# Kernel tuning notes

Hardware: AMD Instinct MI355X
Metric: run time of the kernel (lower is better)

The kernel has to match this reference:

```python
import jax, jax.numpy as jnp
import numpy as np

B, N, DEG = 64, 512, 16        # graphs, nodes per graph, avg degree
C, HID = 10, 128               # input feat dim (== num_classes quirk), hidden
E = B * N * DEG                # total edges (fixed; pooling masks edges)


def _gcn(x, W, b, src, dst, emask, n):
    # PyG GCNConv: add self-loops, symmetric norm D^-1/2 (A+I) D^-1/2 (XW) + b
    h = x @ W
    deg = jax.ops.segment_sum(emask, dst, num_segments=n) + 1.0  # +1 self-loop
    dinv = jax.lax.rsqrt(deg)
    norm = dinv[src] * dinv[dst] * emask
    agg = jax.ops.segment_sum(h[src] * norm[:, None], dst, num_segments=n)
    return agg + h * (dinv * dinv)[:, None] + b  # self-loop term + bias


def _sag_pool(x, src, dst, emask, Wp, bp, n_per):
    # SAGPooling: score = tanh(GCN(x)); per-graph top-k (ratio=0.5); x' = x[perm]*score
    n = x.shape[0]
    score = jnp.tanh(_gcn(x, Wp, bp, src, dst, emask, n)[:, 0])
    k = n_per // 2
    vals, idx = jax.lax.top_k(score.reshape(B, n_per), k)  # [B,k]
    perm = (idx + (jnp.arange(B) * n_per)[:, None]).reshape(-1)
    xk = x[perm] * vals.reshape(-1)[:, None]
    # relabel edges; drop edges touching removed nodes via mask (fixed E)
    mapping = jnp.full((n,), -1, jnp.int32).at[perm].set(
        jnp.arange(B * k, dtype=jnp.int32))
    ns, nd = mapping[src], mapping[dst]
    nmask = emask * ((ns >= 0) & (nd >= 0)).astype(emask.dtype)
    return xk, jnp.maximum(ns, 0), jnp.maximum(nd, 0), nmask, k


def _readout(x, k):
    # global max pool || global mean pool (all kept nodes are real, no padding)
    xg = x.reshape(B, k, -1)
    return jnp.concatenate([xg.max(axis=1), xg.mean(axis=1)], axis=1)


def setup_inputs() -> dict:
    key = jax.random.key(0)
    ks = jax.random.split(key, 16)
    x = jax.random.normal(ks[0], (B * N, C), jnp.float32)
    off = jnp.repeat(jnp.arange(B, dtype=jnp.int32) * N, N * DEG)
    src = jax.random.randint(ks[1], (E,), 0, N, jnp.int32) + off
    dst = jax.random.randint(ks[2], (E,), 0, N, jnp.int32) + off
    p = lambda k, s: jax.random.normal(k, s, jnp.float32) * 0.05
    return {
        "x": x, "src": src, "dst": dst,
        "W1": p(ks[3], (C, HID)), "b1": jnp.zeros((HID,), jnp.float32),
        "W2": p(ks[4], (HID, HID)), "b2": jnp.zeros((HID,), jnp.float32),
        "W3": p(ks[5], (HID, HID)), "b3": jnp.zeros((HID,), jnp.float32),
        "Wp": p(ks[6], (HID, 1)), "bp": jnp.zeros((1,), jnp.float32),
        "L1W": p(ks[7], (2 * HID, HID)), "L1b": jnp.zeros((HID,), jnp.float32),
        "L2W": p(ks[8], (HID, HID // 2)), "L2b": jnp.zeros((HID // 2,), jnp.float32),
    }


def reference(x, src, dst, W1, b1, W2, b2, W3, b3, Wp, bp, L1W, L1b, L2W, L2b):
    emask = jnp.ones((E,), jnp.float32)
    h = jax.nn.relu(_gcn(x, W1, b1, src, dst, emask, B * N))
    h, src, dst, emask, k = _sag_pool(h, src, dst, emask, Wp, bp, N)
    x1 = _readout(h, k)
    h = jax.nn.relu(_gcn(h, W2, b2, src, dst, emask, B * k))
    h, src, dst, emask, k = _sag_pool(h, src, dst, emask, Wp, bp, k)
    x2 = _readout(h, k)
    h = jax.nn.relu(_gcn(h, W3, b3, src, dst, emask, B * k))
    h, src, dst, emask, k = _sag_pool(h, src, dst, emask, Wp, bp, k)
    x3 = _readout(h, k)
    z = x1 + x2 + x3
    z = jax.nn.relu(z @ L1W + L1b)
    # dropout inactive in eval mode
    z = jax.nn.relu(z @ L2W + L2b)
    return jax.nn.log_softmax(z, axis=1)
```

## Files before the change

kernel.cpp:

```cpp
#include <hip/hip_runtime.h>
#include <math.h>

#define BGR 64
#define N0 512
#define E_TOT (BGR*N0*16)
#define EPG 8192
#define EIT 16
#define HID 128


__global__ __launch_bounds__(512) void k_topo0(
    const int* __restrict__ s0, const int* __restrict__ d0,
    int2* __restrict__ edges, int* __restrict__ cnt, int* __restrict__ rowptr,
    float* __restrict__ dinv, int2* __restrict__ csr){
  __shared__ int   deg[512];
  __shared__ int   sb[512];
  __shared__ int   cur[512];
  __shared__ float dl[512];
  int g = (blockIdx.x & 7)*8 + (blockIdx.x >> 3);
  int t = threadIdx.x;
  int gbase = g*N0, ebase = g*EPG;
  deg[t] = 0;
  __syncthreads();
  int2 ebuf[EIT];
  #pragma unroll
  for (int it = 0; it < EIT; it++){
    int i = ebase + it*512 + t;
    int2 e = make_int2(s0[i], d0[i]);
    ebuf[it] = e;
    edges[i] = e;
    atomicAdd(&deg[e.y - gbase], 1);
  }
  __syncthreads();
  int vdeg = deg[t];
  sb[t] = vdeg; __syncthreads();
  for (int off = 1; off < 512; off <<= 1){
    int add = (t >= off) ? sb[t-off] : 0;
    __syncthreads(); sb[t] += add; __syncthreads();
  }
  int excl = sb[t] - vdeg;
  rowptr[gbase + t] = ebase + excl;
  cnt[gbase + t] = vdeg;
  cur[t] = excl;
  float dv = rsqrtf((float)vdeg + 1.f);
  dl[t] = dv;
  dinv[gbase + t] = dv;
  __syncthreads();
  #pragma unroll
  for (int it = 0; it < EIT; it++){
    int2 e = ebuf[it];
    int sl = e.x - gbase, dc = e.y - gbase;
    int pos = atomicAdd(&cur[dc], 1);
    csr[ebase + pos] = make_int2(e.x, __float_as_int(dl[sl]*dl[dc]));
  }
}

__global__ __launch_bounds__(512) void k_l1_fused(
    const float* __restrict__ x, const float* __restrict__ W1,
    const int2* __restrict__ csr, const int* __restrict__ rowptr,
    const int* __restrict__ cnt, const float* __restrict__ dinv,
    const float* __restrict__ b1, const float* __restrict__ Wp,
    float4* __restrict__ gout4, float* __restrict__ hp_part){
  extern __shared__ float hl[];
  int b = blockIdx.x;
  int xcd = b & 7, idx = b >> 3;
  int graph = xcd*8 + (idx >> 3);
  int sub = idx & 7;
  int qf = sub >> 1, half = sub & 1;
  int t = threadIdx.x;
  int gbase = graph*N0;
  int fp = t & 31;
  int f = qf*32 + fp;
  float wcol[10];
  #pragma unroll
  for (int k = 0; k < 10; k++) wcol[k] = W1[k*HID + f];
  for (int n = t >> 5; n < N0; n += 16){
    const float* xr = x + (gbase + n)*10;
    float acc = 0.f;
    #pragma unroll
    for (int k = 0; k < 10; k++) acc += xr[k]*wcol[k];
    hl[n*32 + fp] = acc;
  }
  __syncthreads();
  const float4* hl4 = (const float4*)hl;
  int l = t & 7, grp = t >> 3;
  float4 bb = ((const float4*)b1)[qf*8 + l];
  float4 wp = ((const float4*)Wp)[qf*8 + l];
  int n0 = half*256;
  for (int nl = n0 + grp; nl < n0 + 256; nl += 64){
    int node = gbase + nl;
    int start = rowptr[node], c = cnt[node];
    float4 acc = make_float4(0.f,0.f,0.f,0.f);
    int j = 0;
    for (; j + 4 <= c; j += 4){
      int2 e0 = csr[start+j],   e1 = csr[start+j+1];
      int2 e2 = csr[start+j+2], e3 = csr[start+j+3];
      float4 h0 = hl4[(e0.x - gbase)*8 + l];
      float4 h1 = hl4[(e1.x - gbase)*8 + l];
      float4 h2 = hl4[(e2.x - gbase)*8 + l];
      float4 h3 = hl4[(e3.x - gbase)*8 + l];
      float w0 = __int_as_float(e0.y), w1 = __int_as_float(e1.y);
      float w2 = __int_as_float(e2.y), w3 = __int_as_float(e3.y);
      acc.x += w0*h0.x + w1*h1.x + w2*h2.x + w3*h3.x;
      acc.y += w0*h0.y + w1*h1.y + w2*h2.y + w3*h3.y;
      acc.z += w0*h0.z + w1*h1.z + w2*h2.z + w3*h3.z;
      acc.w += w0*h0.w + w1*h1.w + w2*h2.w + w3*h3.w;
    }
    for (; j < c; j++){
      int2 e = csr[start + j];
      float wgt = __int_as_float(e.y);
      float4 hv = hl4[(e.x - gbase)*8 + l];
      acc.x += wgt*hv.x; acc.y += wgt*hv.y; acc.z += wgt*hv.z; acc.w += wgt*hv.w;
    }
    float di = dinv[node], dd = di*di;
    float4 hs = hl4[nl*8 + l];
    float4 v;
    v.x = fmaxf(acc.x + hs.x*dd + bb.x, 0.f);
    v.y = fmaxf(acc.y + hs.y*dd + bb.y, 0.f);
    v.z = fmaxf(acc.z + hs.z*dd + bb.z, 0.f);
    v.w = fmaxf(acc.w + hs.w*dd + bb.w, 0.f);
    gout4[node*32 + qf*8 + l] = v;
    float contrib = v.x*wp.x + v.y*wp.y + v.z*wp.z + v.w*wp.w;
    #pragma unroll
    for (int off = 4; off; off >>= 1) contrib += __shfl_down(contrib, off, 8);
    if (l == 0) hp_part[qf*32768 + node] = contrib;
  }
}

__global__ void k_gemm16(const float* __restrict__ x, const float* __restrict__ W,
                         float* __restrict__ out, int nper){
  __shared__ float xr[16][HID];
  int b = blockIdx.x;
  int xcd = b & 7, idx = b >> 3, bpg = nper >> 4;
  int graph = xcd*8 + idx / bpg;
  int base = graph*nper + (idx % bpg)*16;
  int f = threadIdx.x;
  #pragma unroll
  for (int nd = 0; nd < 16; nd++) xr[nd][f] = x[(base+nd)*HID + f];
  __syncthreads();
  float acc[16];
  #pragma unroll
  for (int nd = 0; nd < 16; nd++) acc[nd] = 0.f;
  for (int i = 0; i < HID; i++){
    float wv = W[i*HID + f];
    #pragma unroll
    for (int nd = 0; nd < 16; nd++) acc[nd] += xr[nd][i]*wv;
  }
  #pragma unroll
  for (int nd = 0; nd < 16; nd++) out[(base+nd)*HID + f] = acc[nd];
}

__global__ __launch_bounds__(256) void k_gcn_gather(
    const float4* __restrict__ h4, const int2* __restrict__ csr,
    const int* __restrict__ rowptr, const int* __restrict__ cnt,
    const float* __restrict__ dinv, const float4* __restrict__ bias4,
    const float4* __restrict__ Wp4, float4* __restrict__ out4,
    float* __restrict__ hp, int nper){
  int b = blockIdx.x;
  int xcd = b & 7, idx = b >> 3, bpg = nper >> 3;
  int graph = xcd*8 + idx / bpg;
  int node = graph*nper + (idx % bpg)*8 + (threadIdx.x >> 5);
  int l = threadIdx.x & 31;
  int start = rowptr[node], c = cnt[node];
  float4 acc = make_float4(0.f, 0.f, 0.f, 0.f);
  int j = 0;
  for (; j + 4 <= c; j += 4){
    int2 e0 = csr[start+j],   e1 = csr[start+j+1];
    int2 e2 = csr[start+j+2], e3 = csr[start+j+3];
    float4 h0 = h4[e0.x*32 + l];
    float4 h1 = h4[e1.x*32 + l];
    float4 h2 = h4[e2.x*32 + l];
    float4 h3 = h4[e3.x*32 + l];
    float w0 = __int_as_float(e0.y), w1 = __int_as_float(e1.y);
    float w2 = __int_as_float(e2.y), w3 = __int_as_float(e3.y);
    acc.x += w0*h0.x + w1*h1.x + w2*h2.x + w3*h3.x;
    acc.y += w0*h0.y + w1*h1.y + w2*h2.y + w3*h3.y;
    acc.z += w0*h0.z + w1*h1.z + w2*h2.z + w3*h3.z;
    acc.w += w0*h0.w + w1*h1.w + w2*h2.w + w3*h3.w;
  }
  for (; j < c; j++){
    int2 e = csr[start + j];
    float wgt = __int_as_float(e.y);
    float4 hv = h4[e.x*32 + l];
    acc.x += wgt*hv.x; acc.y += wgt*hv.y; acc.z += wgt*hv.z; acc.w += wgt*hv.w;
  }
  float di = dinv[node], dd = di*di;
  float4 hs = h4[node*32 + l];
  float4 bb = bias4[l];
  float4 v;
  v.x = fmaxf(acc.x + hs.x*dd + bb.x, 0.f);
  v.y = fmaxf(acc.y + hs.y*dd + bb.y, 0.f);
  v.z = fmaxf(acc.z + hs.z*dd + bb.z, 0.f);
  v.w = fmaxf(acc.w + hs.w*dd + bb.w, 0.f);
  out4[node*32 + l] = v;
  float4 wp = Wp4[l];
  float contrib = v.x*wp.x + v.y*wp.y + v.z*wp.z + v.w*wp.w;
  #pragma unroll
  for (int off = 16; off; off >>= 1) contrib += __shfl_down(contrib, off, 32);
  if (l == 0) hp[node] = contrib;
}

__global__ __launch_bounds__(512) void k_mega(
    const float4* __restrict__ gout4, const float* __restrict__ hp_part,
    int l1flag, const float* __restrict__ hp,
    int2* __restrict__ csr, int* __restrict__ rowptr, int* __restrict__ cnt,
    float* __restrict__ dinv, const float* __restrict__ bp,
    int2* __restrict__ edges, float4* __restrict__ xpool4,
    float* __restrict__ z, int nper, int lastlev,
    const float* __restrict__ L1W, const float* __restrict__ L1b,
    const float* __restrict__ L2W, const float* __restrict__ L2b,
    float* __restrict__ out){
  __shared__ float sv[512];
  __shared__ int   si[512];
  __shared__ float hpl[512];
  __shared__ int   map[512];
  __shared__ int   sb[512];
  __shared__ int   cur[256];
  __shared__ float dl[256];
  __shared__ float4 pmx[16][32];
  __shared__ float4 psm[16][32];
  __shared__ float zr[256];
  __shared__ float h1[128];
  __shared__ float h2[64];
  __shared__ float red[2];
  int g = (blockIdx.x & 7)*8 + (blockIdx.x >> 3);
  int t = threadIdx.x;
  int k = nper >> 1;
  int gbase = g*nper, ebase = g*EPG, gb2 = g*k;
  bool act = t < nper;
  if (act){
    int node = gbase + t;
    hpl[t] = l1flag ? (hp_part[node] + hp_part[32768 + node] +
                       hp_part[65536 + node] + hp_part[98304 + node])
                    : hp[node];
  }
  __syncthreads();
  float v = 0.f; int idx = t;
  if (act){
    int start = rowptr[gbase + t], c = cnt[gbase + t];
    float a = 0.f;
    int j = 0;
    for (; j + 4 <= c; j += 4){
      int2 e0 = csr[start+j],   e1 = csr[start+j+1];
      int2 e2 = csr[start+j+2], e3 = csr[start+j+3];
      a += __int_as_float(e0.y)*hpl[e0.x - gbase]
         + __int_as_float(e1.y)*hpl[e1.x - gbase]
         + __int_as_float(e2.y)*hpl[e2.x - gbase]
         + __int_as_float(e3.y)*hpl[e3.x - gbase];
    }
    for (; j < c; j++){
      int2 e = csr[start + j];
      a += __int_as_float(e.y)*hpl[e.x - gbase];
    }
    float di = dinv[gbase + t];
    v = tanhf(a + hpl[t]*di*di + bp[0]);
  }
  for (int kk = 2; kk <= nper; kk <<= 1){
    for (int jj = kk >> 1; jj > 0; jj >>= 1){
      if (jj >= 64){
        if (act){ sv[t] = v; si[t] = idx; }
        __syncthreads();
        if (act){
          int p = t ^ jj;
          float pv = sv[p]; int pi = si[p];
          bool amLower = (t & jj) == 0;
          bool dirDesc = (t & kk) == 0;
          bool betterMine = (v > pv) || (v == pv && idx < pi);
          if ((amLower == dirDesc) != betterMine){ v = pv; idx = pi; }
        }
        __syncthreads();
      } else if (act){
        float pv = __shfl_xor(v, jj);
        int   pi = __shfl_xor(idx, jj);
        bool amLower = (t & jj) == 0;
        bool dirDesc = (t & kk) == 0;
        bool betterMine = (v > pv) || (v == pv && idx < pi);
        if ((amLower == dirDesc) != betterMine){ v = pv; idx = pi; }
      }
    }
  }
  if (act){ sv[t] = v; si[t] = idx; }
  __syncthreads();
  int l = t & 31, j0 = t >> 5;
  float4 mx = make_float4(-INFINITY,-INFINITY,-INFINITY,-INFINITY);
  float4 sm = make_float4(0.f,0.f,0.f,0.f);
  for (int j = j0; j < k; j += 16){
    float val = sv[j]; int row = si[j];
    float4 hv = gout4[(gbase + row)*32 + l];
    float4 o = make_float4(hv.x*val, hv.y*val, hv.z*val, hv.w*val);
    if (!lastlev) xpool4[(gb2 + j)*32 + l] = o;
    mx.x = fmaxf(mx.x, o.x); mx.y = fmaxf(mx.y, o.y);
    mx.z = fmaxf(mx.z, o.z); mx.w = fmaxf(mx.w, o.w);
    sm.x += o.x; sm.y += o.y; sm.z += o.z; sm.w += o.w;
  }
  pmx[j0][l] = mx; psm[j0][l] = sm;
  __syncthreads();
  if (t < 32){
    float4 M = pmx[0][t], S = psm[0][t];
    #pragma unroll
    for (int q = 1; q < 16; q++){
      float4 m2 = pmx[q][t], s2 = psm[q][t];
      M.x = fmaxf(M.x, m2.x); M.y = fmaxf(M.y, m2.y);
      M.z = fmaxf(M.z, m2.z); M.w = fmaxf(M.w, m2.w);
      S.x += s2.x; S.y += s2.y; S.z += s2.z; S.w += s2.w;
    }
    float ki = 1.f/(float)k;
    float* zp = z + g*256;
    if (l1flag){
      zp[t*4+0] = M.x; zp[t*4+1] = M.y; zp[t*4+2] = M.z; zp[t*4+3] = M.w;
      zp[128+t*4+0] = S.x*ki; zp[128+t*4+1] = S.y*ki;
      zp[128+t*4+2] = S.z*ki; zp[128+t*4+3] = S.w*ki;
    } else if (!lastlev){
      zp[t*4+0] += M.x; zp[t*4+1] += M.y; zp[t*4+2] += M.z; zp[t*4+3] += M.w;
      zp[128+t*4+0] += S.x*ki; zp[128+t*4+1] += S.y*ki;
      zp[128+t*4+2] += S.z*ki; zp[128+t*4+3] += S.w*ki;
    } else {
      zr[t*4+0] = zp[t*4+0] + M.x; zr[t*4+1] = zp[t*4+1] + M.y;
      zr[t*4+2] = zp[t*4+2] + M.z; zr[t*4+3] = zp[t*4+3] + M.w;
      zr[128+t*4+0] = zp[128+t*4+0] + S.x*ki;
      zr[128+t*4+1] = zp[128+t*4+1] + S.y*ki;
      zr[128+t*4+2] = zp[128+t*4+2] + S.z*ki;
      zr[128+t*4+3] = zp[128+t*4+3] + S.w*ki;
    }
  }
  if (lastlev){
    __syncthreads();
    if (t < 128){
      float a = L1b[t];
      for (int i = 0; i < 256; i++) a += zr[i]*L1W[i*128 + t];
      h1[t] = fmaxf(a, 0.f);
    }
    __syncthreads();
    if (t < 64){
      float a = L2b[t];
      for (int i = 0; i < 128; i++) a += h1[i]*L2W[i*64 + t];
      h2[t] = fmaxf(a, 0.f);
    }
    __syncthreads();
    if (t == 0){
      float mxv = -INFINITY;
      for (int i = 0; i < 64; i++) mxv = fmaxf(mxv, h2[i]);
      float s = 0.f;
      for (int i = 0; i < 64; i++) s += expf(h2[i] - mxv);
      red[0] = mxv; red[1] = logf(s);
    }
    __syncthreads();
    if (t < 64) out[g*64 + t] = h2[t] - red[0] - red[1];
    return;
  }
  if (act) map[t] = -1;
  if (t < k) sb[t] = 0;
  __syncthreads();
  if (t < k) map[si[t]] = t;
  __syncthreads();
  int2 ebuf[EIT];
  #pragma unroll
  for (int it = 0; it < EIT; it++){
    int i = ebase + it*512 + t;
    int2 e = edges[i];
    int2 ne = make_int2(-1, 0);
    if (e.x >= 0){
      int ns = map[e.x - gbase], nd = map[e.y - gbase];
      if (ns >= 0 && nd >= 0){
        ne = make_int2(gb2 + ns, gb2 + nd);
        atomicAdd(&sb[nd], 1);
      }
    }
    ebuf[it] = ne;
    edges[i] = ne;
  }
  __syncthreads();
  int vdeg = (t < k) ? sb[t] : 0;
  for (int off = 1; off < k; off <<= 1){
    int add = (t >= off && t < k) ? sb[t-off] : 0;
    __syncthreads();
    if (t < k) sb[t] += add;
    __syncthreads();
  }
  if (t < k){
    int excl = sb[t] - vdeg;
    rowptr[gb2 + t] = ebase + excl;
    cnt[gb2 + t] = vdeg;
    cur[t] = excl;
    float dv = rsqrtf((float)vdeg + 1.f);
    dl[t] = dv;
    dinv[gb2 + t] = dv;
  }
  __syncthreads();
  #pragma unroll
  for (int it = 0; it < EIT; it++){
    int2 e = ebuf[it];
    if (e.x >= 0){
      int sl = e.x - gb2, dc = e.y - gb2;
      int pos = atomicAdd(&cur[dc], 1);
      csr[ebase + pos] = make_int2(e.x, __float_as_int(dl[sl]*dl[dc]));
    }
  }
}

extern "C" void kernel_launch(void* const* d_in, const int* in_sizes, int n_in,
                              void* d_out, int out_size, void* d_ws, size_t ws_size,
                              hipStream_t stream){
  (void)in_sizes; (void)n_in; (void)out_size; (void)ws_size;
  const float* x0  = (const float*)d_in[0];
  const int*   s0  = (const int*)  d_in[1];
  const int*   d0  = (const int*)  d_in[2];
  const float* W1  = (const float*)d_in[3];  const float* b1 = (const float*)d_in[4];
  const float* W2  = (const float*)d_in[5];  const float* b2 = (const float*)d_in[6];
  const float* W3  = (const float*)d_in[7];  const float* b3 = (const float*)d_in[8];
  const float* Wp  = (const float*)d_in[9];  const float* bp = (const float*)d_in[10];
  const float* L1W = (const float*)d_in[11]; const float* L1b = (const float*)d_in[12];
  const float* L2W = (const float*)d_in[13]; const float* L2b = (const float*)d_in[14];
  float* out = (float*)d_out;

  float* w = (float*)d_ws;
  float* h     = w; w += 32768*HID;
  float* gout  = w; w += 32768*HID;
  float* xpA   = h    + 16384*HID;
  float* xpB   = gout + 16384*HID;
  float* xpC   = xpA;
  float* dinvv = w; w += 32768;
  float* hp    = w; w += 32768;
  float* hppt  = w; w += 4*32768;
  float* z     = w; w += BGR*256;
  int* cnt     = (int*)w; w += 32768;
  int* rowptr  = (int*)w; w += 32768;
  int2* edges  = (int2*)w; w += 2*E_TOT;
  int2* csr    = (int2*)w; w += 2*E_TOT;

  k_topo0<<<BGR, 512, 0, stream>>>(s0, d0, edges, cnt, rowptr, dinvv, csr);

  k_l1_fused<<<512, 512, 65536, stream>>>(x0, W1, csr, rowptr, cnt, dinvv,
                                          b1, Wp, (float4*)gout, hppt);
  k_mega<<<BGR, 512, 0, stream>>>((const float4*)gout, hppt, 1, hp, csr, rowptr,
                                  cnt, dinvv, bp, edges, (float4*)xpA, z, 512, 0,
                                  L1W, L1b, L2W, L2b, out);
  k_gemm16<<<16384/16, HID, 0, stream>>>(xpA, W2, h, 256);
  k_gcn_gather<<<16384/8, 256, 0, stream>>>((const float4*)h, csr, rowptr, cnt,
                                            dinvv, (const float4*)b2,
                                            (const float4*)Wp, (float4*)gout,
                                            hp, 256);
  k_mega<<<BGR, 512, 0, stream>>>((const float4*)gout, hppt, 0, hp, csr, rowptr,
                                  cnt, dinvv, bp, edges, (float4*)xpB, z, 256, 0,
                                  L1W, L1b, L2W, L2b, out);
  k_gemm16<<<8192/16, HID, 0, stream>>>(xpB, W3, h, 128);
  k_gcn_gather<<<8192/8, 256, 0, stream>>>((const float4*)h, csr, rowptr, cnt,
                                           dinvv, (const float4*)b3,
                                           (const float4*)Wp, (float4*)gout,
                                           hp, 128);
  k_mega<<<BGR, 512, 0, stream>>>((const float4*)gout, hppt, 0, hp, csr, rowptr,
                                  cnt, dinvv, bp, edges, (float4*)xpC, z, 128, 1,
                                  L1W, L1b, L2W, L2b, out);
}
```

Baseline: 246.0 us.

## Fuse pooling levels 2-3, GEMMs and readout into one per-graph tail kernel

Replaces the seven launches after layer 1 (three pooling kernels, two GEMMs, two gathers) with one kernel that runs one 512-thread block per graph. Each block keeps pooled features in 128 KB of LDS and does the GEMM, GCN aggregation, scoring, sort, relabel and readout in place, using coherent atomic loads for CSR data it rewrote itself. This removes launch overhead and global round-trips of intermediate features. In exchange only 64 blocks run, so most of the GPU sits idle during the dense GEMM and gather stages, and the large LDS footprint limits occupancy.

Result: slower. 268.0 us (+9.0%).

```diff
diff --git a/kernel.cpp b/kernel.cpp
--- a/kernel.cpp
+++ b/kernel.cpp
@@ -8,6 +8,186 @@
 #define EIT 16
 #define HID 128
 
+
+__device__ __forceinline__ int2 ldcoh(const int2* p){
+  unsigned long long v = __hip_atomic_load(
+      (const unsigned long long*)p, __ATOMIC_RELAXED, __HIP_MEMORY_SCOPE_AGENT);
+  int2 r; r.x = (int)(unsigned int)v; r.y = (int)(unsigned int)(v >> 32);
+  return r;
+}
+
+template<bool COH>
+__device__ __forceinline__ int2 lde(const int2* p){
+  if (COH) return ldcoh(p);
+  return *p;
+}
+
+template<bool COH>
+__device__ __forceinline__ float score_edges(const int2* __restrict__ csr,
+    int start, int c, const float* hloc, int gbase){
+  float a = 0.f; int j = 0;
+  for (; j + 4 <= c; j += 4){
+    int2 e0 = lde<COH>(csr+start+j),   e1 = lde<COH>(csr+start+j+1);
+    int2 e2 = lde<COH>(csr+start+j+2), e3 = lde<COH>(csr+start+j+3);
+    a += __int_as_float(e0.y)*hloc[e0.x - gbase]
+       + __int_as_float(e1.y)*hloc[e1.x - gbase]
+       + __int_as_float(e2.y)*hloc[e2.x - gbase]
+       + __int_as_float(e3.y)*hloc[e3.x - gbase];
+  }
+  for (; j < c; j++){
+    int2 e = lde<COH>(csr+start+j);
+    a += __int_as_float(e.y)*hloc[e.x - gbase];
+  }
+  return a;
+}
+
+__device__ __forceinline__ float4 row_edges_coh(const int2* __restrict__ csr,
+    int start, int c, const float4* h4, int gbase, int l){
+  float4 acc = make_float4(0.f,0.f,0.f,0.f);
+  int j = 0;
+  for (; j + 4 <= c; j += 4){
+    int2 e0 = ldcoh(csr+start+j),   e1 = ldcoh(csr+start+j+1);
+    int2 e2 = ldcoh(csr+start+j+2), e3 = ldcoh(csr+start+j+3);
+    float4 h0 = h4[(e0.x - gbase)*32 + l];
+    float4 h1 = h4[(e1.x - gbase)*32 + l];
+    float4 h2 = h4[(e2.x - gbase)*32 + l];
+    float4 h3 = h4[(e3.x - gbase)*32 + l];
+    float w0 = __int_as_float(e0.y), w1 = __int_as_float(e1.y);
+    float w2 = __int_as_float(e2.y), w3 = __int_as_float(e3.y);
+    acc.x += w0*h0.x + w1*h1.x + w2*h2.x + w3*h3.x;
+    acc.y += w0*h0.y + w1*h1.y + w2*h2.y + w3*h3.y;
+    acc.z += w0*h0.z + w1*h1.z + w2*h2.z + w3*h3.z;
+    acc.w += w0*h0.w + w1*h1.w + w2*h2.w + w3*h3.w;
+  }
+  for (; j < c; j++){
+    int2 e = ldcoh(csr+start+j);
+    float wgt = __int_as_float(e.y);
+    float4 hv = h4[(e.x - gbase)*32 + l];
+    acc.x += wgt*hv.x; acc.y += wgt*hv.y; acc.z += wgt*hv.z; acc.w += wgt*hv.w;
+  }
+  return acc;
+}
+
+__device__ __forceinline__ void bitonic_sort(float* sv, int* si, float v, int idx,
+                                             int t, int nper, bool act){
+  for (int kk = 2; kk <= nper; kk <<= 1){
+    for (int jj = kk >> 1; jj > 0; jj >>= 1){
+      if (jj >= 64){
+        if (act){ sv[t] = v; si[t] = idx; }
+        __syncthreads();
+        if (act){
+          int p = t ^ jj;
+          float pv = sv[p]; int pi = si[p];
+          bool amLower = (t & jj) == 0;
+          bool dirDesc = (t & kk) == 0;
+          bool betterMine = (v > pv) || (v == pv && idx < pi);
+          if ((amLower == dirDesc) != betterMine){ v = pv; idx = pi; }
+        }
+        __syncthreads();
+      } else if (act){
+        float pv = __shfl_xor(v, jj);
+        int   pi = __shfl_xor(idx, jj);
+        bool amLower = (t & jj) == 0;
+        bool dirDesc = (t & kk) == 0;
+        bool betterMine = (v > pv) || (v == pv && idx < pi);
+        if ((amLower == dirDesc) != betterMine){ v = pv; idx = pi; }
+      }
+    }
+  }
+  if (act){ sv[t] = v; si[t] = idx; }
+  __syncthreads();
+}
+
+template<bool COH>
+__device__ __forceinline__ void relabel(int2* __restrict__ edges,
+    int2* __restrict__ csr, const int* si, int* map, int* sb, int* cur,
+    float* dl, int* rpl, int* cntl, int t, int nper, int k,
+    int gbase, int ebase){
+  if (t < nper) map[t] = -1;
+  if (t < k) sb[t] = 0;
+  __syncthreads();
+  if (t < k) map[si[t]] = t;
+  __syncthreads();
+  int2 ebuf[EIT];
+  #pragma unroll
+  for (int it = 0; it < EIT; it++){
+    int i = ebase + it*512 + t;
+    int2 e = lde<COH>(edges + i);
+    int2 ne = make_int2(-1, 0);
+    if (e.x >= 0){
+      int ns = map[e.x - gbase], nd = map[e.y - gbase];
+      if (ns >= 0 && nd >= 0){
+        ne = make_int2(gbase + ns, gbase + nd);
+        atomicAdd(&sb[nd], 1);
+      }
+    }
+    ebuf[it] = ne;
+    edges[i] = ne;
+  }
+  __syncthreads();
+  int vdeg = (t < k) ? sb[t] : 0;
+  for (int off = 1; off < k; off <<= 1){
+    int add = (t >= off && t < k) ? sb[t-off] : 0;
+    __syncthreads();
+    if (t < k) sb[t] += add;
+    __syncthreads();
+  }
+  if (t < k){
+    int excl = sb[t] - vdeg;
+    rpl[t] = ebase + excl;
+    cntl[t] = vdeg;
+    cur[t] = excl;
+    float dv = rsqrtf((float)vdeg + 1.f);
+    dl[t] = dv;
+  }
+  __syncthreads();
+  #pragma unroll
+  for (int it = 0; it < EIT; it++){
+    int2 e = ebuf[it];
+    if (e.x >= 0){
+      int sl = e.x - gbase, dc = e.y - gbase;
+      int pos = atomicAdd(&cur[dc], 1);
+      csr[ebase + pos] = make_int2(e.x, __float_as_int(dl[sl]*dl[dc]));
+    }
+  }
+  __syncthreads();
+}
+
+__device__ __forceinline__ void gemm_inplace(float* xl, const float* __restrict__ W,
+                                             int nn, int t){
+  float4* xl4 = (float4*)xl;
+  int fq = t & 31;
+  int ng = t >> 5;
+  for (int tb = 0; tb < nn; tb += 64){
+    int n0 = tb + ng*4;
+    float4 acc[4];
+    #pragma unroll
+    for (int c = 0; c < 4; c++) acc[c] = make_float4(0.f,0.f,0.f,0.f);
+    for (int i = 0; i < HID; i += 4){
+      float4 w0 = *(const float4*)(W + (i+0)*HID + fq*4);
+      float4 w1 = *(const float4*)(W + (i+1)*HID + fq*4);
+      float4 w2 = *(const float4*)(W + (i+2)*HID + fq*4);
+      float4 w3 = *(const float4*)(W + (i+3)*HID + fq*4);
+      #pragma unroll
+      for (int c = 0; c < 4; c++){
+        float4 xv = *(const float4*)(xl + (n0+c)*HID + i);
+        acc[c].x += xv.x*w0.x; acc[c].x += xv.y*w1.x;
+        acc[c].x += xv.z*w2.x; acc[c].x += xv.w*w3.x;
+        acc[c].y += xv.x*w0.y; acc[c].y += xv.y*w1.y;
+        acc[c].y += xv.z*w2.y; acc[c].y += xv.w*w3.y;
+        acc[c].z += xv.x*w0.z; acc[c].z += xv.y*w1.z;
+        acc[c].z += xv.z*w2.z; acc[c].z += xv.w*w3.z;
+        acc[c].w += xv.x*w0.w; acc[c].w += xv.y*w1.w;
+        acc[c].w += xv.z*w2.w; acc[c].w += xv.w*w3.w;
+      }
+    }
+    __syncthreads();
+    #pragma unroll
+    for (int c = 0; c < 4; c++)
+      xl4[(n0+c)*32 + fq] = acc[c];
+  }
+  __syncthreads();
+}
 
 __global__ __launch_bounds__(512) void k_topo0(
     const int* __restrict__ s0, const int* __restrict__ d0,
@@ -127,275 +307,252 @@
   }
 }
 
-__global__ void k_gemm16(const float* __restrict__ x, const float* __restrict__ W,
-                         float* __restrict__ out, int nper){
-  __shared__ float xr[16][HID];
-  int b = blockIdx.x;
-  int xcd = b & 7, idx = b >> 3, bpg = nper >> 4;
-  int graph = xcd*8 + idx / bpg;
-  int base = graph*nper + (idx % bpg)*16;
-  int f = threadIdx.x;
-  #pragma unroll
-  for (int nd = 0; nd < 16; nd++) xr[nd][f] = x[(base+nd)*HID + f];
-  __syncthreads();
-  float acc[16];
-  #pragma unroll
-  for (int nd = 0; nd < 16; nd++) acc[nd] = 0.f;
-  for (int i = 0; i < HID; i++){
-    float wv = W[i*HID + f];
-    #pragma unroll
-    for (int nd = 0; nd < 16; nd++) acc[nd] += xr[nd][i]*wv;
-  }
-  #pragma unroll
-  for (int nd = 0; nd < 16; nd++) out[(base+nd)*HID + f] = acc[nd];
-}
-
-__global__ __launch_bounds__(256) void k_gcn_gather(
-    const float4* __restrict__ h4, const int2* __restrict__ csr,
-    const int* __restrict__ rowptr, const int* __restrict__ cnt,
-    const float* __restrict__ dinv, const float4* __restrict__ bias4,
-    const float4* __restrict__ Wp4, float4* __restrict__ out4,
-    float* __restrict__ hp, int nper){
-  int b = blockIdx.x;
-  int xcd = b & 7, idx = b >> 3, bpg = nper >> 3;
-  int graph = xcd*8 + idx / bpg;
-  int node = graph*nper + (idx % bpg)*8 + (threadIdx.x >> 5);
-  int l = threadIdx.x & 31;
-  int start = rowptr[node], c = cnt[node];
-  float4 acc = make_float4(0.f, 0.f, 0.f, 0.f);
-  int j = 0;
-  for (; j + 4 <= c; j += 4){
-    int2 e0 = csr[start+j],   e1 = csr[start+j+1];
-    int2 e2 = csr[start+j+2], e3 = csr[start+j+3];
-    float4 h0 = h4[e0.x*32 + l];
-    float4 h1 = h4[e1.x*32 + l];
-    float4 h2 = h4[e2.x*32 + l];
-    float4 h3 = h4[e3.x*32 + l];
-    float w0 = __int_as_float(e0.y), w1 = __int_as_float(e1.y);
-    float w2 = __int_as_float(e2.y), w3 = __int_as_float(e3.y);
-    acc.x += w0*h0.x + w1*h1.x + w2*h2.x + w3*h3.x;
-    acc.y += w0*h0.y + w1*h1.y + w2*h2.y + w3*h3.y;
-    acc.z += w0*h0.z + w1*h1.z + w2*h2.z + w3*h3.z;
-    acc.w += w0*h0.w + w1*h1.w + w2*h2.w + w3*h3.w;
-  }
-  for (; j < c; j++){
-    int2 e = csr[start + j];
-    float wgt = __int_as_float(e.y);
-    float4 hv = h4[e.x*32 + l];
-    acc.x += wgt*hv.x; acc.y += wgt*hv.y; acc.z += wgt*hv.z; acc.w += wgt*hv.w;
-  }
-  float di = dinv[node], dd = di*di;
-  float4 hs = h4[node*32 + l];
-  float4 bb = bias4[l];
-  float4 v;
-  v.x = fmaxf(acc.x + hs.x*dd + bb.x, 0.f);
-  v.y = fmaxf(acc.y + hs.y*dd + bb.y, 0.f);
-  v.z = fmaxf(acc.z + hs.z*dd + bb.z, 0.f);
-  v.w = fmaxf(acc.w + hs.w*dd + bb.w, 0.f);
-  out4[node*32 + l] = v;
-  float4 wp = Wp4[l];
-  float contrib = v.x*wp.x + v.y*wp.y + v.z*wp.z + v.w*wp.w;
-  #pragma unroll
-  for (int off = 16; off; off >>= 1) contrib += __shfl_down(contrib, off, 32);
-  if (l == 0) hp[node] = contrib;
-}
-
-__global__ __launch_bounds__(512) void k_mega(
+__global__ __launch_bounds__(512) void k_tail(
     const float4* __restrict__ gout4, const float* __restrict__ hp_part,
-    int l1flag, const float* __restrict__ hp,
-    int2* __restrict__ csr, int* __restrict__ rowptr, int* __restrict__ cnt,
-    float* __restrict__ dinv, const float* __restrict__ bp,
-    int2* __restrict__ edges, float4* __restrict__ xpool4,
-    float* __restrict__ z, int nper, int lastlev,
+    int2* __restrict__ csr, int2* __restrict__ edges,
+    const int* __restrict__ rowptr1, const int* __restrict__ cnt1,
+    const float* __restrict__ dinv1, const float* __restrict__ bp,
+    const float* __restrict__ W2, const float* __restrict__ b2,
+    const float* __restrict__ W3, const float* __restrict__ b3,
+    const float* __restrict__ Wp,
     const float* __restrict__ L1W, const float* __restrict__ L1b,
     const float* __restrict__ L2W, const float* __restrict__ L2b,
     float* __restrict__ out){
+  __shared__ float xl[256*HID];
   __shared__ float sv[512];
   __shared__ int   si[512];
   __shared__ float hpl[512];
-  __shared__ int   map[512];
-  __shared__ int   sb[512];
-  __shared__ int   cur[256];
+  __shared__ union UU {
+    struct { int map[512]; int sb[512]; int cur[256]; } r;
+    float4 pr[2][16][32];
+  } u;
   __shared__ float dl[256];
-  __shared__ float4 pmx[16][32];
-  __shared__ float4 psm[16][32];
-  __shared__ float zr[256];
-  __shared__ float h1[128];
-  __shared__ float h2[64];
+  __shared__ int   rpl[256];
+  __shared__ int   cntl[256];
+  __shared__ float zacc[256];
   __shared__ float red[2];
+
   int g = (blockIdx.x & 7)*8 + (blockIdx.x >> 3);
   int t = threadIdx.x;
-  int k = nper >> 1;
-  int gbase = g*nper, ebase = g*EPG, gb2 = g*k;
-  bool act = t < nper;
-  if (act){
+  int gbase = g*N0, ebase = g*EPG;
+  int l = t & 31, j0 = t >> 5;
+  float4* xl4 = (float4*)xl;
+  float bp0 = bp[0];
+
+  {
     int node = gbase + t;
-    hpl[t] = l1flag ? (hp_part[node] + hp_part[32768 + node] +
-                       hp_part[65536 + node] + hp_part[98304 + node])
-                    : hp[node];
-  }
-  __syncthreads();
-  float v = 0.f; int idx = t;
-  if (act){
-    int start = rowptr[gbase + t], c = cnt[gbase + t];
-    float a = 0.f;
-    int j = 0;
-    for (; j + 4 <= c; j += 4){
-      int2 e0 = csr[start+j],   e1 = csr[start+j+1];
-      int2 e2 = csr[start+j+2], e3 = csr[start+j+3];
-      a += __int_as_float(e0.y)*hpl[e0.x - gbase]
-         + __int_as_float(e1.y)*hpl[e1.x - gbase]
-         + __int_as_float(e2.y)*hpl[e2.x - gbase]
-         + __int_as_float(e3.y)*hpl[e3.x - gbase];
-    }
-    for (; j < c; j++){
-      int2 e = csr[start + j];
-      a += __int_as_float(e.y)*hpl[e.x - gbase];
-    }
-    float di = dinv[gbase + t];
-    v = tanhf(a + hpl[t]*di*di + bp[0]);
-  }
-  for (int kk = 2; kk <= nper; kk <<= 1){
-    for (int jj = kk >> 1; jj > 0; jj >>= 1){
-      if (jj >= 64){
-        if (act){ sv[t] = v; si[t] = idx; }
-        __syncthreads();
-        if (act){
-          int p = t ^ jj;
-          float pv = sv[p]; int pi = si[p];
-          bool amLower = (t & jj) == 0;
-          bool dirDesc = (t & kk) == 0;
-          bool betterMine = (v > pv) || (v == pv && idx < pi);
-          if ((amLower == dirDesc) != betterMine){ v = pv; idx = pi; }
-        }
-        __syncthreads();
-      } else if (act){
-        float pv = __shfl_xor(v, jj);
-        int   pi = __shfl_xor(idx, jj);
-        bool amLower = (t & jj) == 0;
-        bool dirDesc = (t & kk) == 0;
-        bool betterMine = (v > pv) || (v == pv && idx < pi);
-        if ((amLower == dirDesc) != betterMine){ v = pv; idx = pi; }
+    hpl[t] = hp_part[node] + hp_part[32768 + node]
+           + hp_part[65536 + node] + hp_part[98304 + node];
+  }
+  __syncthreads();
+  {
+    int start = rowptr1[gbase + t], c = cnt1[gbase + t];
+    float a = score_edges<false>(csr, start, c, hpl, gbase);
+    float di = dinv1[gbase + t];
+    float v = tanhf(a + hpl[t]*di*di + bp0);
+    bitonic_sort(sv, si, v, t, t, 512, true);
+  }
+  {
+    float4 mx = make_float4(-INFINITY,-INFINITY,-INFINITY,-INFINITY);
+    float4 sm = make_float4(0.f,0.f,0.f,0.f);
+    for (int j = j0; j < 256; j += 16){
+      float val = sv[j]; int row = si[j];
+      float4 hv = gout4[(gbase + row)*32 + l];
+      float4 o = make_float4(hv.x*val, hv.y*val, hv.z*val, hv.w*val);
+      xl4[j*32 + l] = o;
+      mx.x = fmaxf(mx.x, o.x); mx.y = fmaxf(mx.y, o.y);
+      mx.z = fmaxf(mx.z, o.z); mx.w = fmaxf(mx.w, o.w);
+      sm.x += o.x; sm.y += o.y; sm.z += o.z; sm.w += o.w;
+    }
+    u.pr[0][j0][l] = mx; u.pr[1][j0][l] = sm;
+    __syncthreads();
+    if (t < 32){
+      float4 M = u.pr[0][0][t], S = u.pr[1][0][t];
+      #pragma unroll
+      for (int q = 1; q < 16; q++){
+        float4 m2 = u.pr[0][q][t], s2 = u.pr[1][q][t];
+        M.x = fmaxf(M.x, m2.x); M.y = fmaxf(M.y, m2.y);
+        M.z = fmaxf(M.z, m2.z); M.w = fmaxf(M.w, m2.w);
+        S.x += s2.x; S.y += s2.y; S.z += s2.z; S.w += s2.w;
       }
-    }
-  }
-  if (act){ sv[t] = v; si[t] = idx; }
-  __syncthreads();
-  int l = t & 31, j0 = t >> 5;
-  float4 mx = make_float4(-INFINITY,-INFINITY,-INFINITY,-INFINITY);
-  float4 sm = make_float4(0.f,0.f,0.f,0.f);
-  for (int j = j0; j < k; j += 16){
-    float val = sv[j]; int row = si[j];
-    float4 hv = gout4[(gbase + row)*32 + l];
-    float4 o = make_float4(hv.x*val, hv.y*val, hv.z*val, hv.w*val);
-    if (!lastlev) xpool4[(gb2 + j)*32 + l] = o;
-    mx.x = fmaxf(mx.x, o.x); mx.y = fmaxf(mx.y, o.y);
-    mx.z = fmaxf(mx.z, o.z); mx.w = fmaxf(mx.w, o.w);
-    sm.x += o.x; sm.y += o.y; sm.z += o.z; sm.w += o.w;
-  }
-  pmx[j0][l] = mx; psm[j0][l] = sm;
-  __syncthreads();
-  if (t < 32){
-    float4 M = pmx[0][t], S = psm[0][t];
-    #pragma unroll
-    for (int q = 1; q < 16; q++){
-      float4 m2 = pmx[q][t], s2 = psm[q][t];
-      M.x = fmaxf(M.x, m2.x); M.y = fmaxf(M.y, m2.y);
-      M.z = fmaxf(M.z, m2.z); M.w = fmaxf(M.w, m2.w);
-      S.x += s2.x; S.y += s2.y; S.z += s2.z; S.w += s2.w;
-    }
-    float ki = 1.f/(float)k;
-    float* zp = z + g*256;
-    if (l1flag){
-      zp[t*4+0] = M.x; zp[t*4+1] = M.y; zp[t*4+2] = M.z; zp[t*4+3] = M.w;
-      zp[128+t*4+0] = S.x*ki; zp[128+t*4+1] = S.y*ki;
-      zp[128+t*4+2] = S.z*ki; zp[128+t*4+3] = S.w*ki;
-    } else if (!lastlev){
-      zp[t*4+0] += M.x; zp[t*4+1] += M.y; zp[t*4+2] += M.z; zp[t*4+3] += M.w;
-      zp[128+t*4+0] += S.x*ki; zp[128+t*4+1] += S.y*ki;
-      zp[128+t*4+2] += S.z*ki; zp[128+t*4+3] += S.w*ki;
-    } else {
-      zr[t*4+0] = zp[t*4+0] + M.x; zr[t*4+1] = zp[t*4+1] + M.y;
-      zr[t*4+2] = zp[t*4+2] + M.z; zr[t*4+3] = zp[t*4+3] + M.w;
-      zr[128+t*4+0] = zp[128+t*4+0] + S.x*ki;
-      zr[128+t*4+1] = zp[128+t*4+1] + S.y*ki;
-      zr[128+t*4+2] = zp[128+t*4+2] + S.z*ki;
-      zr[128+t*4+3] = zp[128+t*4+3] + S.w*ki;
-    }
-  }
-  if (lastlev){
-    __syncthreads();
+      float ki = 1.f/256.f;
+      zacc[t*4+0] = M.x; zacc[t*4+1] = M.y; zacc[t*4+2] = M.z; zacc[t*4+3] = M.w;
+      zacc[128+t*4+0] = S.x*ki; zacc[128+t*4+1] = S.y*ki;
+      zacc[128+t*4+2] = S.z*ki; zacc[128+t*4+3] = S.w*ki;
+    }
+    __syncthreads();
+  }
+  relabel<false>(edges, csr, si, u.r.map, u.r.sb, u.r.cur, dl, rpl, cntl,
+                 t, 512, 256, gbase, ebase);
+
+  gemm_inplace(xl, W2, 256, t);
+  {
+    float4 bb = ((const float4*)b2)[l];
+    float4 wp = ((const float4*)Wp)[l];
+    for (int r = 0; r < 16; r++){
+      int n = r*16 + j0;
+      float4 acc = row_edges_coh(csr, rpl[n], cntl[n], xl4, gbase, l);
+      float di = dl[n], dd = di*di;
+      float4 hs = xl4[n*32 + l];
+      float4 v;
+      v.x = fmaxf(acc.x + hs.x*dd + bb.x, 0.f);
+      v.y = fmaxf(acc.y + hs.y*dd + bb.y, 0.f);
+      v.z = fmaxf(acc.z + hs.z*dd + bb.z, 0.f);
+      v.w = fmaxf(acc.w + hs.w*dd + bb.w, 0.f);
+      float contrib = v.x*wp.x + v.y*wp.y + v.z*wp.z + v.w*wp.w;
+      #pragma unroll
+      for (int off = 16; off; off >>= 1) contrib += __shfl_down(contrib, off, 32);
+      if (l == 0) hpl[n] = contrib;
+    }
+  }
+  __syncthreads();
+
+  {
+    float v = 0.f;
+    if (t < 256){
+      float a = score_edges<true>(csr, rpl[t], cntl[t], hpl, gbase);
+      float di = dl[t];
+      v = tanhf(a + hpl[t]*di*di + bp0);
+    }
+    bitonic_sort(sv, si, v, t, t, 256, t < 256);
+  }
+  {
+    float4 bb = ((const float4*)b2)[l];
+    float4 o[8];
+    float4 mx = make_float4(-INFINITY,-INFINITY,-INFINITY,-INFINITY);
+    float4 sm = make_float4(0.f,0.f,0.f,0.f);
+    #pragma unroll
+    for (int r = 0; r < 8; r++){
+      int j = j0 + 16*r;
+      float val = sv[j]; int row = si[j];
+      float4 acc = row_edges_coh(csr, rpl[row], cntl[row], xl4, gbase, l);
+      float di = dl[row], dd = di*di;
+      float4 hs = xl4[row*32 + l];
+      float4 v;
+      v.x = fmaxf(acc.x + hs.x*dd + bb.x, 0.f);
+      v.y = fmaxf(acc.y + hs.y*dd + bb.y, 0.f);
+      v.z = fmaxf(acc.z + hs.z*dd + bb.z, 0.f);
+      v.w = fmaxf(acc.w + hs.w*dd + bb.w, 0.f);
+      float4 ov = make_float4(v.x*val, v.y*val, v.z*val, v.w*val);
+      o[r] = ov;
+      mx.x = fmaxf(mx.x, ov.x); mx.y = fmaxf(mx.y, ov.y);
+      mx.z = fmaxf(mx.z, ov.z); mx.w = fmaxf(mx.w, ov.w);
+      sm.x += ov.x; sm.y += ov.y; sm.z += ov.z; sm.w += ov.w;
+    }
+    u.pr[0][j0][l] = mx; u.pr[1][j0][l] = sm;
+    __syncthreads();
+    #pragma unroll
+    for (int r = 0; r < 8; r++){ int j = j0 + 16*r; xl4[j*32 + l] = o[r]; }
+    if (t < 32){
+      float4 M = u.pr[0][0][t], S = u.pr[1][0][t];
+      #pragma unroll
+      for (int q = 1; q < 16; q++){
+        float4 m2 = u.pr[0][q][t], s2 = u.pr[1][q][t];
+        M.x = fmaxf(M.x, m2.x); M.y = fmaxf(M.y, m2.y);
+        M.z = fmaxf(M.z, m2.z); M.w = fmaxf(M.w, m2.w);
+        S.x += s2.x; S.y += s2.y; S.z += s2.z; S.w += s2.w;
+      }
+      float ki = 1.f/128.f;
+      zacc[t*4+0] += M.x; zacc[t*4+1] += M.y; zacc[t*4+2] += M.z; zacc[t*4+3] += M.w;
+      zacc[128+t*4+0] += S.x*ki; zacc[128+t*4+1] += S.y*ki;
+      zacc[128+t*4+2] += S.z*ki; zacc[128+t*4+3] += S.w*ki;
+    }
+    __syncthreads();
+  }
+  relabel<true>(edges, csr, si, u.r.map, u.r.sb, u.r.cur, dl, rpl, cntl,
+                t, 256, 128, gbase, ebase);
+
+  gemm_inplace(xl, W3, 128, t);
+  {
+    float4 bb = ((const float4*)b3)[l];
+    float4 wp = ((const float4*)Wp)[l];
+    for (int r = 0; r < 8; r++){
+      int n = r*16 + j0;
+      float4 acc = row_edges_coh(csr, rpl[n], cntl[n], xl4, gbase, l);
+      float di = dl[n], dd = di*di;
+      float4 hs = xl4[n*32 + l];
+      float4 v;
+      v.x = fmaxf(acc.x + hs.x*dd + bb.x, 0.f);
+      v.y = fmaxf(acc.y + hs.y*dd + bb.y, 0.f);
+      v.z = fmaxf(acc.z + hs.z*dd + bb.z, 0.f);
+      v.w = fmaxf(acc.w + hs.w*dd + bb.w, 0.f);
+      float contrib = v.x*wp.x + v.y*wp.y + v.z*wp.z + v.w*wp.w;
+      #pragma unroll
+      for (int off = 16; off; off >>= 1) contrib += __shfl_down(contrib, off, 32);
+      if (l == 0) hpl[n] = contrib;
+    }
+  }
+  __syncthreads();
+
+  {
+    float v = 0.f;
     if (t < 128){
-      float a = L1b[t];
-      for (int i = 0; i < 256; i++) a += zr[i]*L1W[i*128 + t];
-      h1[t] = fmaxf(a, 0.f);
-    }
-    __syncthreads();
-    if (t < 64){
-      float a = L2b[t];
-      for (int i = 0; i < 128; i++) a += h1[i]*L2W[i*64 + t];
-      h2[t] = fmaxf(a, 0.f);
-    }
-    __syncthreads();
-    if (t == 0){
-      float mxv = -INFINITY;
-      for (int i = 0; i < 64; i++) mxv = fmaxf(mxv, h2[i]);
-      float s = 0.f;
-      for (int i = 0; i < 64; i++) s += expf(h2[i] - mxv);
-      red[0] = mxv; red[1] = logf(s);
-    }
-    __syncthreads();
-    if (t < 64) out[g*64 + t] = h2[t] - red[0] - red[1];
-    return;
-  }
-  if (act) map[t] = -1;
-  if (t < k) sb[t] = 0;
-  __syncthreads();
-  if (t < k) map[si[t]] = t;
-  __syncthreads();
-  int2 ebuf[EIT];
-  #pragma unroll
-  for (int it = 0; it < EIT; it++){
-    int i = ebase + it*512 + t;
-    int2 e = edges[i];
-    int2 ne = make_int2(-1, 0);
-    if (e.x >= 0){
-      int ns = map[e.x - gbase], nd = map[e.y - gbase];
-      if (ns >= 0 && nd >= 0){
-        ne = make_int2(gb2 + ns, gb2 + nd);
-        atomicAdd(&sb[nd], 1);
+      float a = score_edges<true>(csr, rpl[t], cntl[t], hpl, gbase);
+      float di = dl[t];
+      v = tanhf(a + hpl[t]*di*di + bp0);
+    }
+    bitonic_sort(sv, si, v, t, t, 128, t < 128);
+  }
+  {
+    float4 bb = ((const float4*)b3)[l];
+    float4 mx = make_float4(-INFINITY,-INFINITY,-INFINITY,-INFINITY);
+    float4 sm = make_float4(0.f,0.f,0.f,0.f);
+    #pragma unroll
+    for (int r = 0; r < 4; r++){
+      int j = j0 + 16*r;
+      float val = sv[j]; int row = si[j];
+      float4 acc = row_edges_coh(csr, rpl[row], cntl[row], xl4, gbase, l);
+      float di = dl[row], dd = di*di;
+      float4 hs = xl4[row*32 + l];
+      float4 v;
+      v.x = fmaxf(acc.x + hs.x*dd + bb.x, 0.f);
+      v.y = fmaxf(acc.y + hs.y*dd + bb.y, 0.f);
+      v.z = fmaxf(acc.z + hs.z*dd + bb.z, 0.f);
+      v.w = fmaxf(acc.w + hs.w*dd + bb.w, 0.f);
+      float4 ov = make_float4(v.x*val, v.y*val, v.z*val, v.w*val);
+      mx.x = fmaxf(mx.x, ov.x); mx.y = fmaxf(mx.y, ov.y);
+      mx.z = fmaxf(mx.z, ov.z); mx.w = fmaxf(mx.w, ov.w);
+      sm.x += ov.x; sm.y += ov.y; sm.z += ov.z; sm.w += ov.w;
+    }
+    u.pr[0][j0][l] = mx; u.pr[1][j0][l] = sm;
+    __syncthreads();
+    if (t < 32){
+      float4 M = u.pr[0][0][t], S = u.pr[1][0][t];
+      #pragma unroll
+      for (int q = 1; q < 16; q++){
+        float4 m2 = u.pr[0][q][t], s2 = u.pr[1][q][t];
+        M.x = fmaxf(M.x, m2.x); M.y = fmaxf(M.y, m2.y);
+        M.z = fmaxf(M.z, m2.z); M.w = fmaxf(M.w, m2.w);
+        S.x += s2.x; S.y += s2.y; S.z += s2.z; S.w += s2.w;
       }
-    }
-    ebuf[it] = ne;
-    edges[i] = ne;
-  }
-  __syncthreads();
-  int vdeg = (t < k) ? sb[t] : 0;
-  for (int off = 1; off < k; off <<= 1){
-    int add = (t >= off && t < k) ? sb[t-off] : 0;
-    __syncthreads();
-    if (t < k) sb[t] += add;
-    __syncthreads();
-  }
-  if (t < k){
-    int excl = sb[t] - vdeg;
-    rowptr[gb2 + t] = ebase + excl;
-    cnt[gb2 + t] = vdeg;
-    cur[t] = excl;
-    float dv = rsqrtf((float)vdeg + 1.f);
-    dl[t] = dv;
-    dinv[gb2 + t] = dv;
-  }
-  __syncthreads();
-  #pragma unroll
-  for (int it = 0; it < EIT; it++){
-    int2 e = ebuf[it];
-    if (e.x >= 0){
-      int sl = e.x - gb2, dc = e.y - gb2;
-      int pos = atomicAdd(&cur[dc], 1);
-      csr[ebase + pos] = make_int2(e.x, __float_as_int(dl[sl]*dl[dc]));
-    }
-  }
+      float ki = 1.f/64.f;
+      zacc[t*4+0] += M.x; zacc[t*4+1] += M.y; zacc[t*4+2] += M.z; zacc[t*4+3] += M.w;
+      zacc[128+t*4+0] += S.x*ki; zacc[128+t*4+1] += S.y*ki;
+      zacc[128+t*4+2] += S.z*ki; zacc[128+t*4+3] += S.w*ki;
+    }
+    __syncthreads();
+  }
+  if (t < 128){
+    float a = L1b[t];
+    for (int i = 0; i < 256; i++) a += zacc[i]*L1W[i*128 + t];
+    sv[t] = fmaxf(a, 0.f);
+  }
+  __syncthreads();
+  if (t < 64){
+    float a = L2b[t];
+    for (int i = 0; i < 128; i++) a += sv[i]*L2W[i*64 + t];
+    hpl[t] = fmaxf(a, 0.f);
+  }
+  __syncthreads();
+  if (t == 0){
+    float mxv = -INFINITY;
+    for (int i = 0; i < 64; i++) mxv = fmaxf(mxv, hpl[i]);
+    float s = 0.f;
+    for (int i = 0; i < 64; i++) s += expf(hpl[i] - mxv);
+    red[0] = mxv; red[1] = logf(s);
+  }
+  __syncthreads();
+  if (t < 64) out[g*64 + t] = hpl[t] - red[0] - red[1];
 }
 
 extern "C" void kernel_launch(void* const* d_in, const int* in_sizes, int n_in,
@@ -414,41 +571,18 @@
   float* out = (float*)d_out;
 
   float* w = (float*)d_ws;
-  float* h     = w; w += 32768*HID;
   float* gout  = w; w += 32768*HID;
-  float* xpA   = h    + 16384*HID;
-  float* xpB   = gout + 16384*HID;
-  float* xpC   = xpA;
   float* dinvv = w; w += 32768;
-  float* hp    = w; w += 32768;
   float* hppt  = w; w += 4*32768;
-  float* z     = w; w += BGR*256;
   int* cnt     = (int*)w; w += 32768;
   int* rowptr  = (int*)w; w += 32768;
   int2* edges  = (int2*)w; w += 2*E_TOT;
   int2* csr    = (int2*)w; w += 2*E_TOT;
 
   k_topo0<<<BGR, 512, 0, stream>>>(s0, d0, edges, cnt, rowptr, dinvv, csr);
-
   k_l1_fused<<<512, 512, 65536, stream>>>(x0, W1, csr, rowptr, cnt, dinvv,
                                           b1, Wp, (float4*)gout, hppt);
-  k_mega<<<BGR, 512, 0, stream>>>((const float4*)gout, hppt, 1, hp, csr, rowptr,
-                                  cnt, dinvv, bp, edges, (float4*)xpA, z, 512, 0,
+  k_tail<<<BGR, 512, 0, stream>>>((const float4*)gout, hppt, csr, edges,
+                                  rowptr, cnt, dinvv, bp, W2, b2, W3, b3, Wp,
                                   L1W, L1b, L2W, L2b, out);
-  k_gemm16<<<16384/16, HID, 0, stream>>>(xpA, W2, h, 256);
-  k_gcn_gather<<<16384/8, 256, 0, stream>>>((const float4*)h, csr, rowptr, cnt,
-                                            dinvv, (const float4*)b2,
-                                            (const float4*)Wp, (float4*)gout,
-                                            hp, 256);
-  k_mega<<<BGR, 512, 0, stream>>>((const float4*)gout, hppt, 0, hp, csr, rowptr,
-                                  cnt, dinvv, bp, edges, (float4*)xpB, z, 256, 0,
-                                  L1W, L1b, L2W, L2b, out);
-  k_gemm16<<<8192/16, HID, 0, stream>>>(xpB, W3, h, 128);
-  k_gcn_gather<<<8192/8, 256, 0, stream>>>((const float4*)h, csr, rowptr, cnt,
-                                           dinvv, (const float4*)b3,
-                                           (const float4*)Wp, (float4*)gout,
-                                           hp, 128);
-  k_mega<<<BGR, 512, 0, stream>>>((const float4*)gout, hppt, 0, hp, csr, rowptr,
-                                  cnt, dinvv, bp, edges, (float4*)xpC, z, 128, 1,
-                                  L1W, L1b, L2W, L2b, out);
-}
+}
```
